# Performance work log

Hardware: AMD Instinct MI355X
Metric: run time of the kernel (lower is better)

The kernel has to match this reference:

```python
import jax, jax.numpy as jnp
import numpy as np

_SAMPLING_EPS = 1e-5
BIG_NEG = jnp.float32(-1e30)  # finite stand-in for -inf (exact 0 after softmax in fp32)


def setup_inputs() -> dict:
    key = jax.random.key(0)
    ks = jax.random.split(key, 12)
    B, V, P, O, S = 128, 128000, 2048, 256, 4
    return {
        "logits": jax.random.normal(ks[0], (B, V), jnp.float32) * 4.0,
        "prompt_token_ids": jax.random.randint(ks[1], (B, P), 0, V),
        "output_token_ids": jax.random.randint(ks[2], (B, O), 0, V),
        "stop_token_ids": jax.random.randint(ks[3], (B, S), 0, V),
        "min_tokens": jax.random.randint(ks[4], (B,), 0, 512),
        "presence_penalties": jax.random.uniform(ks[5], (B,), jnp.float32),
        "frequency_penalties": jax.random.uniform(ks[6], (B,), jnp.float32),
        "repetition_penalties": 1.0 + 0.3 * jax.random.uniform(ks[7], (B,), jnp.float32),
        "temperature": 0.5 + jax.random.uniform(ks[8], (B,), jnp.float32),
        "top_k": jax.random.randint(ks[9], (B,), 32, 64),
        "top_p": 0.5 + 0.5 * jax.random.uniform(ks[10], (B,), jnp.float32),
        "uniform_noise": jax.random.uniform(ks[11], (B, V), jnp.float32, minval=1e-10, maxval=1.0),
        "max_num_logprobs": 20,
    }


def reference(logits, prompt_token_ids, output_token_ids, stop_token_ids,
              min_tokens, presence_penalties, frequency_penalties,
              repetition_penalties, temperature, top_k, top_p,
              uniform_noise, max_num_logprobs):
    B, V = logits.shape
    x = logits.astype(jnp.float32)
    rows = jnp.arange(B)[:, None]

    # ---- min-token penalty: set stop-token logits to -inf while len(output) < min_tokens
    need = min_tokens > output_token_ids.shape[1]                  # [B]
    stop_pen = jnp.where(need[:, None], BIG_NEG, jnp.inf)          # [B,S]
    x = x.at[rows, stop_token_ids].min(stop_pen)

    # ---- presence / frequency / repetition penalties (vLLM apply_penalties)
    counts = jnp.zeros((B, V), jnp.float32).at[rows, output_token_ids].add(1.0)
    prompt_mask = jnp.zeros((B, V), bool).at[rows, prompt_token_ids].set(True)
    output_mask = counts > 0
    rp = repetition_penalties[:, None]
    penalized = jnp.where(x > 0, x / rp, x * rp)
    x = jnp.where(prompt_mask | output_mask, penalized, x)
    x = x - frequency_penalties[:, None] * counts \
          - presence_penalties[:, None] * output_mask.astype(jnp.float32)

    # ---- temperature (greedy rows: temp treated as 1.0)
    t = jnp.where(temperature < _SAMPLING_EPS, 1.0, temperature)
    x = x / t[:, None]

    # ---- top-k / top-p filtering (per-row k and p)
    order = jnp.argsort(-x, axis=-1)                               # descending
    srt = jnp.take_along_axis(x, order, axis=-1)
    pos = jnp.arange(V)[None, :]
    k_eff = jnp.where(top_k < 1, V, top_k)
    keep_k = pos < k_eff[:, None]
    probs_s = jax.nn.softmax(srt, axis=-1)
    cum = jnp.cumsum(probs_s, axis=-1)
    keep_p = (cum - probs_s) < top_p[:, None]                      # cumulative mass before token < p
    keep = jnp.zeros((B, V), bool).at[rows, order].set(keep_k & keep_p)
    x = jnp.where(keep, x, BIG_NEG)

    orig_logits = x
    # source applies temperature a second time before the final sample
    x2 = x / t[:, None]

    # ---- sample: Gumbel-max random sampling, greedy where temperature ~ 0
    gumbel = -jnp.log(-jnp.log(uniform_noise))
    random_sampled = jnp.argmax(x2 + gumbel, axis=-1)
    greedy_sampled = jnp.argmax(x2, axis=-1)
    sampled = jnp.where(temperature < _SAMPLING_EPS, greedy_sampled,
                        random_sampled).astype(jnp.int32)

    # ---- top-k logprobs
    logprobs = jax.nn.log_softmax(orig_logits, axis=-1)
    topk_logprobs, topk_indices = jax.lax.top_k(logprobs, max_num_logprobs)
    return sampled, topk_logprobs, topk_indices.astype(jnp.int32)
```

## Files before the change

### kernel.cpp

```cpp
#include <hip/hip_runtime.h>
#include <math.h>

#define VV 128000
#define NB 128
#define PP 2048
#define OO 256

#define S   8
#define CH  16000
#define CW  500
#define NT1 512
#define CAP 512
#define HS1 512

#define NT2 256

#define BIG_NEG_F (-1e30f)
#define PAD_KEY 0x007FFFFF80000000ULL
#define LOG2E 1.4426950408889634f

__device__ __forceinline__ unsigned long long packkey(float f, int idx) {
  unsigned int b = __float_as_uint(f);
  unsigned int mf = (b & 0x80000000u) ? ~b : (b | 0x80000000u);
  return ((unsigned long long)mf << 32) | (unsigned long long)(unsigned int)(~(unsigned int)idx);
}
__device__ __forceinline__ float unpack_val(unsigned long long k) {
  unsigned int mf = (unsigned int)(k >> 32);
  unsigned int b = (mf & 0x80000000u) ? (mf & 0x7fffffffu) : ~mf;
  return __uint_as_float(b);
}
__device__ __forceinline__ int unpack_idx(unsigned long long k) {
  return (int)(~(unsigned int)(k & 0xffffffffu));
}

__device__ __forceinline__ float wave_sort64_desc(float v, int lane) {
  for (int k = 2; k <= 64; k <<= 1) {
    for (int j = k >> 1; j > 0; j >>= 1) {
      float o = __shfl_xor(v, j, 64);
      bool smaller = (lane & j) == 0;
      bool dir = (lane & k) == 0;
      v = (smaller == dir) ? fmaxf(v, o) : fminf(v, o);
    }
  }
  return v;
}
__device__ __forceinline__ unsigned long long wave_sort64_desc_u64(unsigned long long v, int lane) {
  for (int k = 2; k <= 64; k <<= 1) {
    for (int j = k >> 1; j > 0; j >>= 1) {
      unsigned long long o = __shfl_xor(v, j, 64);
      bool smaller = (lane & j) == 0;
      bool dir = (lane & k) == 0;
      unsigned long long mx = (v > o) ? v : o;
      unsigned long long mn = (v > o) ? o : v;
      v = (smaller == dir) ? mx : mn;
    }
  }
  return v;
}
__device__ __forceinline__ unsigned long long merge_top64(unsigned long long v,
                                                          const unsigned long long* B,
                                                          int lane) {
  unsigned long long b = B[63 - lane];
  v = (v > b) ? v : b;
  for (int j = 32; j > 0; j >>= 1) {
    unsigned long long o = __shfl_xor(v, j, 64);
    bool hi = (lane & j) == 0;
    unsigned long long mx = (v > o) ? v : o;
    unsigned long long mn = (v > o) ? o : v;
    v = hi ? mx : mn;
  }
  return v;
}

__global__ __launch_bounds__(NT1, 4)
void k_main(const float* __restrict__ logits,
            const int* __restrict__ prompt_ids,
            const int* __restrict__ output_ids,
            const int* __restrict__ stop_ids,
            const int* __restrict__ min_tokens,
            const float* __restrict__ presence_p,
            const float* __restrict__ frequency_p,
            const float* __restrict__ repetition_p,
            const float* __restrict__ temperature,
            float* __restrict__ ws_sum,
            unsigned long long* __restrict__ ws_top)
{
#pragma clang fp contract(off)
  __shared__ unsigned int pbits[CW];
  __shared__ unsigned int obits[CW];
  __shared__ int hkey[HS1];
  __shared__ int hval[HS1];
  __shared__ unsigned long long cand[CAP];
  __shared__ unsigned long long mbuf[4 * 64];
  __shared__ float wtau[NT1 / 64];
  __shared__ float wsum[NT1 / 64];
  __shared__ float tau_sh;
  __shared__ int cnt_sh;

  const int chunk = blockIdx.x;
  const int row   = blockIdx.y;
  const int tid   = threadIdx.x;
  const int lane  = tid & 63;
  const int wv    = tid >> 6;
  const int base  = chunk * CH;

  const float fp  = frequency_p[row];
  const float pp  = presence_p[row];
  const float rp  = repetition_p[row];
  const float inv_rp = 1.0f / rp;
  const float tmp = temperature[row];
  const float t   = (tmp < 1e-5f) ? 1.0f : tmp;
  const float c2  = LOG2E / t;
  const bool need = min_tokens[row] > OO;
  const int s0 = stop_ids[row * 4 + 0];
  const int s1 = stop_ids[row * 4 + 1];
  const int s2 = stop_ids[row * 4 + 2];
  const int s3 = stop_ids[row * 4 + 3];
  const bool anystop = need &&
      (((unsigned)(s0 - base) < CH) || ((unsigned)(s1 - base) < CH) ||
       ((unsigned)(s2 - base) < CH) || ((unsigned)(s3 - base) < CH));

  const float* __restrict__ lrow = logits + (size_t)row * VV + base;
  const int l0 = (0 * NT1 + tid) << 3;
  const int l1 = (1 * NT1 + tid) << 3;
  const int l2 = (2 * NT1 + tid) << 3;
  const int l3 = (3 * NT1 + tid) << 3;
  const bool v3 = l3 < CH;

  float4 A0 = *(const float4*)(lrow + l0);
  float4 B0 = *(const float4*)(lrow + l0 + 4);
  float4 A1 = *(const float4*)(lrow + l1);
  float4 B1 = *(const float4*)(lrow + l1 + 4);
  float4 A2 = *(const float4*)(lrow + l2);
  float4 B2 = *(const float4*)(lrow + l2 + 4);
  float4 A3, B3;
  if (v3) { A3 = *(const float4*)(lrow + l3); B3 = *(const float4*)(lrow + l3 + 4); }

  for (int i = tid; i < CW; i += NT1) { pbits[i] = 0u; obits[i] = 0u; }
  for (int i = tid; i < HS1; i += NT1) { hkey[i] = -1; hval[i] = 0; }
  if (tid == 0) cnt_sh = 0;
  __syncthreads();

  const int4* pr4 = (const int4*)(prompt_ids + (size_t)row * PP);
  for (int i = tid; i < PP / 4; i += NT1) {
    int4 tv = pr4[i];
    int l;
    l = tv.x - base; if ((unsigned)l < CH) atomicOr(&pbits[l >> 5], 1u << (l & 31));
    l = tv.y - base; if ((unsigned)l < CH) atomicOr(&pbits[l >> 5], 1u << (l & 31));
    l = tv.z - base; if ((unsigned)l < CH) atomicOr(&pbits[l >> 5], 1u << (l & 31));
    l = tv.w - base; if ((unsigned)l < CH) atomicOr(&pbits[l >> 5], 1u << (l & 31));
  }
  for (int i = tid; i < OO; i += NT1) {
    int tok = output_ids[row * OO + i];
    int l = tok - base;
    if ((unsigned)l < CH) {
      atomicOr(&obits[l >> 5], 1u << (l & 31));
      unsigned int h = ((unsigned int)tok * 2654435761u) >> 23;
      for (;;) {
        int k = hkey[h];
        if (k == tok) { atomicAdd(&hval[h], 1); break; }
        if (k == -1) {
          int prev = atomicCAS(&hkey[h], -1, tok);
          if (prev == -1 || prev == tok) { atomicAdd(&hval[h], 1); break; }
          continue;
        }
        h = (h + 1) & (HS1 - 1);
      }
    }
  }

  unsigned int stopmask = 0u;
  if (anystop) {
    const int sids[4] = {s0, s1, s2, s3};
#pragma unroll
    for (int q = 0; q < 4; ++q) {
      int local = sids[q] - base;
      if ((unsigned)local < CH) {
        int grp = (local >> 3) / NT1;
        int tt  = (local >> 3) % NT1;
        if (tt == tid) stopmask |= 1u << (grp * 8 + (local & 7));
      }
    }
  }
  __syncthreads();

  float px0[8], px1[8], px2[8], px3[8];
  float gm0 = -INFINITY, gm1 = -INFINITY, gm2 = -INFINITY, gm3 = -INFINITY;
  float esum = 0.0f;

  auto processA = [&](int li, float4 xa, float4 xb, float (&px)[8],
                      float& gm, unsigned int sm8) {
    unsigned int w  = (unsigned)li >> 5;
    unsigned int sh = (unsigned)li & 31u;
    unsigned int pm8 = (pbits[w] >> sh) & 255u;
    unsigned int om8 = (obits[w] >> sh) & 255u;
    float xs[8] = {xa.x, xa.y, xa.z, xa.w, xb.x, xb.y, xb.z, xb.w};
    if (sm8) {
#pragma unroll
      for (int e = 0; e < 8; ++e)
        if ((sm8 >> e) & 1u) xs[e] = BIG_NEG_F;
    }
#pragma unroll
    for (int e = 0; e < 8; ++e) {
      float xp = xs[e];
      float xe = xp;
      if ((pm8 | om8) & (1u << e)) {
        float xa_ = (xp > 0.0f) ? (xp * inv_rp) : (xp * rp);
        float xd_ = (xp > 0.0f) ? (xp / rp)     : (xp * rp);
        if ((om8 >> e) & 1u) {
          int v = base + li + e;
          float cnt = 0.0f;
          unsigned int h = ((unsigned int)v * 2654435761u) >> 23;
          for (;;) {
            int k = hkey[h];
            if (k == -1) break;
            if (k == v) { cnt = (float)hval[h]; break; }
            h = (h + 1) & (HS1 - 1);
          }
          xa_ = xa_ - fp * cnt - pp;
          xd_ = xd_ - fp * cnt - pp;
        }
        esum += exp2f(xa_ * c2);
        xe = xd_;
      } else {
        esum += exp2f(xp * c2);
      }
      gm = fmaxf(gm, xe);
      px[e] = xe;
    }
  };

  processA(l0, A0, B0, px0, gm0, stopmask & 255u);
  processA(l1, A1, B1, px1, gm1, (stopmask >> 8) & 255u);
  processA(l2, A2, B2, px2, gm2, (stopmask >> 16) & 255u);
  if (v3) processA(l3, A3, B3, px3, gm3, (stopmask >> 24) & 255u);

  float mx = fmaxf(fmaxf(gm0, gm1), fmaxf(gm2, gm3));

  float ss = esum;
#pragma unroll
  for (int off = 32; off > 0; off >>= 1) ss += __shfl_down(ss, off, 64);
  if (lane == 0) wsum[wv] = ss;

  float srt = wave_sort64_desc(mx, lane);
  if (lane == 7) wtau[wv] = srt;
  __syncthreads();

  if (tid == 0) {
    float tau = wtau[0];
#pragma unroll
    for (int w = 1; w < NT1 / 64; ++w) tau = fminf(tau, wtau[w]);
    tau_sh = tau;
    float sacc = 0.0f;
#pragma unroll
    for (int w = 0; w < NT1 / 64; ++w) sacc += wsum[w];
    ws_sum[row * S + chunk] = sacc;
  }
  __syncthreads();
  const float taueff = tau_sh;

  auto processB = [&](int li, const float (&px)[8], float gmv) {
    if (gmv < taueff) return;
#pragma unroll
    for (int e = 0; e < 8; ++e) {
      float xe = px[e];
      if (xe >= taueff) {
        float xd = xe / t;
        int p = atomicAdd(&cnt_sh, 1);
        if (p < CAP) cand[p] = packkey(xd, base + li + e);
      }
    }
  };

  processB(l0, px0, gm0);
  processB(l1, px1, gm1);
  processB(l2, px2, gm2);
  if (v3) processB(l3, px3, gm3);

  __syncthreads();
  int total = cnt_sh; if (total > CAP) total = CAP;
  for (int i = tid; i < CAP; i += NT1)
    if (i >= total) cand[i] = PAD_KEY;
  __syncthreads();

  int runs = (total + 63) >> 6; if (runs < 1) runs = 1;
  if (wv < runs) {
    unsigned long long rv = wave_sort64_desc_u64(cand[(wv << 6) + lane], lane);
    cand[(wv << 6) + lane] = rv;
  }
  __syncthreads();

  unsigned long long* outp = &ws_top[((size_t)row * S + chunk) * 64 + lane];
  if (runs > 4) {
    if (wv < 4) {
      unsigned long long a = cand[((2 * wv) << 6) + lane];
      a = merge_top64(a, &cand[(2 * wv + 1) << 6], lane);
      mbuf[(wv << 6) + lane] = a;
    }
    __syncthreads();
    if (wv < 2) {
      unsigned long long a = mbuf[((2 * wv) << 6) + lane];
      a = merge_top64(a, &mbuf[(2 * wv + 1) << 6], lane);
      cand[(wv << 6) + lane] = a;
    }
    __syncthreads();
    if (wv == 0) {
      unsigned long long a = cand[lane];
      a = merge_top64(a, &cand[64], lane);
      *outp = a;
    }
  } else if (runs > 2) {
    if (wv < 2) {
      unsigned long long a = cand[((2 * wv) << 6) + lane];
      a = merge_top64(a, &cand[(2 * wv + 1) << 6], lane);
      mbuf[(wv << 6) + lane] = a;
    }
    __syncthreads();
    if (wv == 0) {
      unsigned long long a = mbuf[lane];
      a = merge_top64(a, &mbuf[64], lane);
      *outp = a;
    }
  } else if (runs == 2) {
    if (wv == 0) {
      unsigned long long a = cand[lane];
      a = merge_top64(a, &cand[64], lane);
      *outp = a;
    }
  } else {
    if (wv == 0) *outp = cand[lane];
  }
}

__global__ __launch_bounds__(NT2)
void k2_finalize(const float* __restrict__ temperature,
                 const int* __restrict__ top_k,
                 const float* __restrict__ top_p,
                 const float* __restrict__ noise,
                 const unsigned long long* __restrict__ ws_top,
                 const float* __restrict__ ws_sum,
                 float* __restrict__ out, int K)
{
#pragma clang fp contract(off)
  __shared__ unsigned long long buf[S * 64];
  __shared__ unsigned long long mbuf[4 * 64];
  __shared__ float sv[64];
  __shared__ int   si[64];
  __shared__ float se[64];
  __shared__ float gv[64];

  const int row  = blockIdx.x;
  const int tid  = threadIdx.x;
  const int lane = tid & 63;
  const int wv   = tid >> 6;

  const float tmp = temperature[row];
  const float t   = (tmp < 1e-5f) ? 1.0f : tmp;
  const int   tk  = top_k[row];
  const float tpv = top_p[row];

  for (int i = tid; i < S * 64; i += NT2)
    buf[i] = ws_top[(size_t)row * S * 64 + i];
  __syncthreads();

  {
    unsigned long long a = buf[((2 * wv) << 6) + lane];
    a = merge_top64(a, &buf[(2 * wv + 1) << 6], lane);
    mbuf[(wv << 6) + lane] = a;
  }
  __syncthreads();
  if (wv < 2) {
    unsigned long long a = mbuf[((2 * wv) << 6) + lane];
    a = merge_top64(a, &mbuf[(2 * wv + 1) << 6], lane);
    buf[(wv << 6) + lane] = a;
  }
  __syncthreads();
  if (wv == 0) {
    unsigned long long a = buf[lane];
    a = merge_top64(a, &buf[64], lane);
    float val = unpack_val(a);
    int   idx = unpack_idx(a);
    float m = __shfl(val, 0, 64);
    sv[lane] = val;
    si[lane] = idx;
    bool ok = (unsigned)idx < VV;
    float u = ok ? noise[(size_t)row * VV + idx] : 0.5f;
    float g = -logf(-logf(u));
    se[lane] = expf(val - m);
    gv[lane] = val / t + g;
  }
  __syncthreads();

  if (tid == 0) {
    float Ssum = 0.0f;
    for (int c = 0; c < S; c++) Ssum += ws_sum[row * S + c];
    const float m = sv[0];
    const float Z = Ssum * exp2f(-m * LOG2E);

    int keff = (tk < 1) ? 64 : (tk < 64 ? tk : 64);

    float cum = 0.0f;
    int nk = 0;
    for (int j = 0; j < 64; j++) {
      if (j >= keff) break;
      if (!(cum < tpv)) break;
      nk++;
      cum += se[j] / Z;
    }

    float Zk = 0.0f;
    for (int j = 0; j < nk; j++) Zk += se[j];
    const float logZk = logf(Zk);

    float bv = -INFINITY; int bi = 0x7fffffff;
    for (int j = 0; j < nk; j++) {
      float val = gv[j];
      if (val > bv || (val == bv && si[j] < bi)) { bv = val; bi = si[j]; }
    }
    const int samp = (tmp < 1e-5f) ? si[0] : bi;
    out[row] = (float)samp;

    unsigned long long bm0 = 0ull, bm1 = 0ull;
    for (int j = 0; j < nk; j++) {
      int ix = si[j];
      if (ix < 64) bm0 |= 1ull << ix;
      else if (ix < 128) bm1 |= 1ull << (ix - 64);
    }
    int fi = 0;
    for (int j = 0; j < K; j++) {
      float lp; int ix;
      if (j < nk) {
        lp = (sv[j] - m) - logZk;
        ix = si[j];
      } else {
        while ((fi < 64) ? ((bm0 >> fi) & 1ull) : ((bm1 >> (fi - 64)) & 1ull)) fi++;
        ix = fi; fi++;
        lp = BIG_NEG_F;
      }
      out[NB + row * K + j]            = lp;
      out[NB + NB * K + row * K + j]   = (float)ix;
    }
  }
}

extern "C" void kernel_launch(void* const* d_in, const int* in_sizes, int n_in,
                              void* d_out, int out_size, void* d_ws, size_t ws_size,
                              hipStream_t stream) {
  const float* logits = (const float*)d_in[0];
  const int*   prompt = (const int*)d_in[1];
  const int*   outids = (const int*)d_in[2];
  const int*   stop   = (const int*)d_in[3];
  const int*   mint   = (const int*)d_in[4];
  const float* pres   = (const float*)d_in[5];
  const float* freq   = (const float*)d_in[6];
  const float* rep    = (const float*)d_in[7];
  const float* temp   = (const float*)d_in[8];
  const int*   topk   = (const int*)d_in[9];
  const float* topp   = (const float*)d_in[10];
  const float* noise  = (const float*)d_in[11];

  int B_ = in_sizes[4];
  int K_ = (out_size - B_) / (2 * B_);

  float* ws_sum = (float*)d_ws;
  unsigned long long* ws_top = (unsigned long long*)(ws_sum + (size_t)NB * S);

  dim3 g1(S, B_);
  k_main<<<g1, NT1, 0, stream>>>(logits, prompt, outids, stop, mint,
                                 pres, freq, rep, temp, ws_sum, ws_top);
  k2_finalize<<<B_, NT2, 0, stream>>>(temp, topk, topp, noise,
                                      ws_top, ws_sum, (float*)d_out, K_);
}
```

Baseline: 196.3 us.

## Fuse finalize kernel into main via last-block-per-row atomic counter

Merges the per-row finalize kernel into the main chunk kernel. Each chunk block publishes its partial sum and top-64 with agent-scope atomic stores, then bumps a per-row counter, and the last block to arrive merges the chunks and computes sampling and logprobs. This removes the second kernel launch and its dependency gap. It adds a memset launch and runs the final merge on a single wave instead of a whole block.

```diff
diff --git a/kernel.cpp b/kernel.cpp
--- a/kernel.cpp
+++ b/kernel.cpp
@@ -13,8 +13,6 @@
 #define CAP 512
 #define HS1 512
 
-#define NT2 256
-
 #define BIG_NEG_F (-1e30f)
 #define PAD_KEY 0x007FFFFF80000000ULL
 #define LOG2E 1.4426950408889634f
@@ -31,6 +29,19 @@
 }
 __device__ __forceinline__ int unpack_idx(unsigned long long k) {
   return (int)(~(unsigned int)(k & 0xffffffffu));
+}
+
+__device__ __forceinline__ void st_coh_u64(unsigned long long* p, unsigned long long v) {
+  __hip_atomic_store(p, v, __ATOMIC_RELAXED, __HIP_MEMORY_SCOPE_AGENT);
+}
+__device__ __forceinline__ unsigned long long ld_coh_u64(const unsigned long long* p) {
+  return __hip_atomic_load(p, __ATOMIC_RELAXED, __HIP_MEMORY_SCOPE_AGENT);
+}
+__device__ __forceinline__ void st_coh_f32(float* p, float v) {
+  __hip_atomic_store(p, v, __ATOMIC_RELAXED, __HIP_MEMORY_SCOPE_AGENT);
+}
+__device__ __forceinline__ float ld_coh_f32(const float* p) {
+  return __hip_atomic_load(p, __ATOMIC_RELAXED, __HIP_MEMORY_SCOPE_AGENT);
 }
 
 __device__ __forceinline__ float wave_sort64_desc(float v, int lane) {
@@ -73,17 +84,22 @@
 }
 
 __global__ __launch_bounds__(NT1, 4)
-void k_main(const float* __restrict__ logits,
-            const int* __restrict__ prompt_ids,
-            const int* __restrict__ output_ids,
-            const int* __restrict__ stop_ids,
-            const int* __restrict__ min_tokens,
-            const float* __restrict__ presence_p,
-            const float* __restrict__ frequency_p,
-            const float* __restrict__ repetition_p,
-            const float* __restrict__ temperature,
-            float* __restrict__ ws_sum,
-            unsigned long long* __restrict__ ws_top)
+void k_all(const float* __restrict__ logits,
+           const int* __restrict__ prompt_ids,
+           const int* __restrict__ output_ids,
+           const int* __restrict__ stop_ids,
+           const int* __restrict__ min_tokens,
+           const float* __restrict__ presence_p,
+           const float* __restrict__ frequency_p,
+           const float* __restrict__ repetition_p,
+           const float* __restrict__ temperature,
+           const int* __restrict__ top_k,
+           const float* __restrict__ top_p,
+           const float* __restrict__ noise,
+           int* __restrict__ ws_cnt,
+           float* __restrict__ ws_sum,
+           unsigned long long* __restrict__ ws_top,
+           float* __restrict__ out, int K)
 {
 #pragma clang fp contract(off)
   __shared__ unsigned int pbits[CW];
@@ -96,6 +112,10 @@
   __shared__ float wsum[NT1 / 64];
   __shared__ float tau_sh;
   __shared__ int cnt_sh;
+  __shared__ float sv[64];
+  __shared__ int   si[64];
+  __shared__ float se[64];
+  __shared__ float gv[64];
 
   const int chunk = blockIdx.x;
   const int row   = blockIdx.y;
@@ -254,7 +274,7 @@
     float sacc = 0.0f;
 #pragma unroll
     for (int w = 0; w < NT1 / 64; ++w) sacc += wsum[w];
-    ws_sum[row * S + chunk] = sacc;
+    st_coh_f32(&ws_sum[row * S + chunk], sacc);
   }
   __syncthreads();
   const float taueff = tau_sh;
@@ -307,7 +327,7 @@
     if (wv == 0) {
       unsigned long long a = cand[lane];
       a = merge_top64(a, &cand[64], lane);
-      *outp = a;
+      st_coh_u64(outp, a);
     }
   } else if (runs > 2) {
     if (wv < 2) {
@@ -319,65 +339,39 @@
     if (wv == 0) {
       unsigned long long a = mbuf[lane];
       a = merge_top64(a, &mbuf[64], lane);
-      *outp = a;
+      st_coh_u64(outp, a);
     }
   } else if (runs == 2) {
     if (wv == 0) {
       unsigned long long a = cand[lane];
       a = merge_top64(a, &cand[64], lane);
-      *outp = a;
+      st_coh_u64(outp, a);
     }
   } else {
-    if (wv == 0) *outp = cand[lane];
-  }
-}
-
-__global__ __launch_bounds__(NT2)
-void k2_finalize(const float* __restrict__ temperature,
-                 const int* __restrict__ top_k,
-                 const float* __restrict__ top_p,
-                 const float* __restrict__ noise,
-                 const unsigned long long* __restrict__ ws_top,
-                 const float* __restrict__ ws_sum,
-                 float* __restrict__ out, int K)
-{
-#pragma clang fp contract(off)
-  __shared__ unsigned long long buf[S * 64];
-  __shared__ unsigned long long mbuf[4 * 64];
-  __shared__ float sv[64];
-  __shared__ int   si[64];
-  __shared__ float se[64];
-  __shared__ float gv[64];
-
-  const int row  = blockIdx.x;
-  const int tid  = threadIdx.x;
-  const int lane = tid & 63;
-  const int wv   = tid >> 6;
-
-  const float tmp = temperature[row];
-  const float t   = (tmp < 1e-5f) ? 1.0f : tmp;
+    if (wv == 0) st_coh_u64(outp, cand[lane]);
+  }
+
+  if (wv != 0) return;
+  asm volatile("s_waitcnt vmcnt(0)" ::: "memory");
+  int lastv = 0;
+  if (lane == 0) lastv = atomicAdd(&ws_cnt[row], 1);
+  lastv = __shfl(lastv, 0, 64);
+  if (lastv != S - 1) return;
+  asm volatile("" ::: "memory");
+
   const int   tk  = top_k[row];
   const float tpv = top_p[row];
 
-  for (int i = tid; i < S * 64; i += NT2)
-    buf[i] = ws_top[(size_t)row * S * 64 + i];
-  __syncthreads();
+#pragma unroll
+  for (int c = 0; c < S; ++c)
+    cand[(c << 6) + lane] = ld_coh_u64(&ws_top[((size_t)row * S + c) * 64 + lane]);
+
+  unsigned long long a = cand[lane];
+#pragma unroll
+  for (int c = 1; c < S; ++c)
+    a = merge_top64(a, &cand[c << 6], lane);
 
   {
-    unsigned long long a = buf[((2 * wv) << 6) + lane];
-    a = merge_top64(a, &buf[(2 * wv + 1) << 6], lane);
-    mbuf[(wv << 6) + lane] = a;
-  }
-  __syncthreads();
-  if (wv < 2) {
-    unsigned long long a = mbuf[((2 * wv) << 6) + lane];
-    a = merge_top64(a, &mbuf[(2 * wv + 1) << 6], lane);
-    buf[(wv << 6) + lane] = a;
-  }
-  __syncthreads();
-  if (wv == 0) {
-    unsigned long long a = buf[lane];
-    a = merge_top64(a, &buf[64], lane);
     float val = unpack_val(a);
     int   idx = unpack_idx(a);
     float m = __shfl(val, 0, 64);
@@ -389,11 +383,10 @@
     se[lane] = expf(val - m);
     gv[lane] = val / t + g;
   }
-  __syncthreads();
-
-  if (tid == 0) {
+
+  if (lane == 0) {
     float Ssum = 0.0f;
-    for (int c = 0; c < S; c++) Ssum += ws_sum[row * S + c];
+    for (int c = 0; c < S; c++) Ssum += ld_coh_f32(&ws_sum[row * S + c]);
     const float m = sv[0];
     const float Z = Ssum * exp2f(-m * LOG2E);
 
@@ -462,12 +455,13 @@
   int B_ = in_sizes[4];
   int K_ = (out_size - B_) / (2 * B_);
 
-  float* ws_sum = (float*)d_ws;
+  int* ws_cnt = (int*)d_ws;
+  float* ws_sum = (float*)(ws_cnt + NB);
   unsigned long long* ws_top = (unsigned long long*)(ws_sum + (size_t)NB * S);
 
+  hipMemsetAsync(ws_cnt, 0, NB * sizeof(int), stream);
   dim3 g1(S, B_);
-  k_main<<<g1, NT1, 0, stream>>>(logits, prompt, outids, stop, mint,
-                                 pres, freq, rep, temp, ws_sum, ws_top);
-  k2_finalize<<<B_, NT2, 0, stream>>>(temp, topk, topp, noise,
-                                      ws_top, ws_sum, (float*)d_out, K_);
-}
+  k_all<<<g1, NT1, 0, stream>>>(logits, prompt, outids, stop, mint,
+                                pres, freq, rep, temp, topk, topp, noise,
+                                ws_cnt, ws_sum, ws_top, (float*)d_out, K_);
+}
```

After: 200.4 us. 1.02x slower.
